# Kernel tuning notes

Measured on AMD Instinct MI355X. Metric: run time of the kernel, lower is better.

Reference implementation:

```python
import jax, jax.numpy as jnp
import numpy as np
import math

D_MODEL = 1024
N_HEADS = 16
D_K = D_MODEL // N_HEADS
BS, SQ, SK = 2, 2048, 2048


def setup_inputs() -> dict:
    key = jax.random.key(0)
    ks = jax.random.split(key, 7)
    q = jax.random.normal(ks[0], (BS, SQ, D_MODEL), dtype=jnp.float32)
    k = jax.random.normal(ks[1], (BS, SK, D_MODEL), dtype=jnp.float32)
    v = jax.random.normal(ks[2], (BS, SK, D_MODEL), dtype=jnp.float32)
    # causal mask: True = masked out (matches torch masked_fill semantics)
    mask = jnp.broadcast_to(
        ~jnp.tril(jnp.ones((SQ, SK), dtype=bool)), (BS, SQ, SK))
    scale = 1.0 / math.sqrt(D_MODEL)
    wq = jax.random.normal(ks[3], (D_MODEL, D_MODEL), dtype=jnp.float32) * scale
    wk = jax.random.normal(ks[4], (D_MODEL, D_MODEL), dtype=jnp.float32) * scale
    wv = jax.random.normal(ks[5], (D_MODEL, D_MODEL), dtype=jnp.float32) * scale
    wo = jax.random.normal(ks[6], (D_MODEL, D_MODEL), dtype=jnp.float32) * scale
    return {"q": q, "k": k, "v": v, "mask": mask,
            "wq": wq, "wk": wk, "wv": wv, "wo": wo}


def reference(q, k, v, mask, wq, wk, wv, wo):
    bs, sq, _ = q.shape
    sk = k.shape[1]
    # nn.Linear(bias=False): x @ W.T ; reshape to heads -> [b, h, s, d_k]
    qh = (q @ wq.T).reshape(bs, sq, N_HEADS, D_K).transpose(0, 2, 1, 3)
    kh = (k @ wk.T).reshape(bs, sk, N_HEADS, D_K).transpose(0, 2, 1, 3)
    vh = (v @ wv.T).reshape(bs, sk, N_HEADS, D_K).transpose(0, 2, 1, 3)
    # scaled dot-product attention, full [b,h,sq,sk] scores (as original)
    z = jnp.einsum('bhqd,bhkd->bhqk', qh, kh) / math.sqrt(D_K)
    z = jnp.where(mask[:, None, :, :], jnp.float32(-1e10), z)
    z = jax.nn.softmax(z, axis=-1)
    z = jnp.einsum('bhqk,bhkd->bhqd', z, vh)
    z = z.transpose(0, 2, 1, 3).reshape(bs, sq, D_MODEL)
    return z @ wo.T
```

## Files before the change

### kernel.cpp

```cpp
#include <hip/hip_runtime.h>
#include <hip/hip_bf16.h>
#include <stdint.h>

typedef short s16x8 __attribute__((ext_vector_type(8)));
typedef float f32x4 __attribute__((ext_vector_type(4)));

#define BSZ 2
#define SQL 2048
#define DMODEL 1024
#define NHEAD 16
#define DKH 64

#if __has_builtin(__builtin_amdgcn_exp2f)
#define EXP2(x) __builtin_amdgcn_exp2f(x)
#else
#define EXP2(x) exp2f(x)
#endif

__device__ __forceinline__ ushort f2bf(float f) {
  uint32_t u = __float_as_uint(f);
  u += 0x7fffu + ((u >> 16) & 1u);
  return (ushort)(u >> 16);
}

__device__ __forceinline__ uint32_t cvtpk_bf16(float lo, float hi) {
  uint32_t r;
  asm("v_cvt_pk_bf16_f32 %0, %1, %2" : "=v"(r) : "v"(lo), "v"(hi));
  return r;
}

__device__ __forceinline__ float rowmax16(float x) {
  x = fmaxf(x, __int_as_float(__builtin_amdgcn_update_dpp(0, __float_as_int(x), 0x121, 0xf, 0xf, true)));
  x = fmaxf(x, __int_as_float(__builtin_amdgcn_update_dpp(0, __float_as_int(x), 0x122, 0xf, 0xf, true)));
  x = fmaxf(x, __int_as_float(__builtin_amdgcn_update_dpp(0, __float_as_int(x), 0x124, 0xf, 0xf, true)));
  x = fmaxf(x, __int_as_float(__builtin_amdgcn_update_dpp(0, __float_as_int(x), 0x128, 0xf, 0xf, true)));
  return x;
}

__device__ __forceinline__ void gload_lds16(const ushort* g, ushort* l) {
  __builtin_amdgcn_global_load_lds((const __attribute__((address_space(1))) void*)g,
                                   (__attribute__((address_space(3))) void*)l,
                                   16, 0, 0);
}

__global__ void cvt_all(const float* __restrict__ q, const float* __restrict__ k,
                        const float* __restrict__ v, const float* __restrict__ wq,
                        const float* __restrict__ wk, const float* __restrict__ wv,
                        const float* __restrict__ wo, ushort* __restrict__ dq,
                        ushort* __restrict__ dk, ushort* __restrict__ dv,
                        ushort* __restrict__ dwq, ushort* __restrict__ dwk,
                        ushort* __restrict__ dwv, ushort* __restrict__ dwo) {
  int b = blockIdx.x;
  const float* s; ushort* d; int off;
  if (b < 4096)       { s = q;  d = dq;  off = b; }
  else if (b < 8192)  { s = k;  d = dk;  off = b - 4096; }
  else if (b < 12288) { s = v;  d = dv;  off = b - 8192; }
  else if (b < 13312) { s = wq; d = dwq; off = b - 12288; }
  else if (b < 14336) { s = wk; d = dwk; off = b - 13312; }
  else if (b < 15360) { s = wv; d = dwv; off = b - 14336; }
  else                { s = wo; d = dwo; off = b - 15360; }
  int i = (off * 256 + threadIdx.x) * 4;
  float4 x = *(const float4*)(s + i);
  ushort4 o;
  o.x = f2bf(x.x); o.y = f2bf(x.y); o.z = f2bf(x.z); o.w = f2bf(x.w);
  *(ushort4*)(d + i) = o;
}

__device__ __forceinline__ void gemm_core(const ushort* __restrict__ A,
                                          const ushort* __restrict__ B,
                                          ushort* sA, ushort* sB, f32x4 (&acc)[4][4]) {
  const int t = threadIdx.x, w = t >> 6, lane = t & 63;
  const int lrow = lane & 15, lk = (lane >> 4) * 8;
  const int m0 = blockIdx.x * 128, n0 = blockIdx.y * 128;
  const int wm = (w >> 1) * 64, wn = (w & 1) * 64;

  auto stage = [&](int kt, int buf) {
#pragma unroll
    for (int i = 0; i < 2; ++i) {
      int ci = i * 256 + t;
      int row = ci >> 2;
      int ce = (ci & 3) * 8;
      gload_lds16(A + (size_t)(m0 + row) * 1024 + kt * 32 + ce,
                  sA + buf * 4096 + (i * 256 + w * 64) * 8);
      gload_lds16(B + (size_t)(n0 + row) * 1024 + kt * 32 + ce,
                  sB + buf * 4096 + (i * 256 + w * 64) * 8);
    }
  };

  stage(0, 0);
  for (int kt = 0; kt < 32; ++kt) {
    const int cur = kt & 1;
    if (kt < 31) {
      stage(kt + 1, cur ^ 1);
      asm volatile("s_waitcnt vmcnt(4)" ::: "memory");
    } else {
      asm volatile("s_waitcnt vmcnt(0)" ::: "memory");
    }
    __builtin_amdgcn_s_barrier();
    __builtin_amdgcn_sched_barrier(0);
    const ushort* pA = sA + cur * 4096;
    const ushort* pB = sB + cur * 4096;
    s16x8 af[4], bfr[4];
#pragma unroll
    for (int mi = 0; mi < 4; ++mi)
      af[mi] = *(const s16x8*)(pA + (wm + mi * 16 + lrow) * 32 + lk);
#pragma unroll
    for (int ni = 0; ni < 4; ++ni)
      bfr[ni] = *(const s16x8*)(pB + (wn + ni * 16 + lrow) * 32 + lk);
    __builtin_amdgcn_s_setprio(1);
#pragma unroll
    for (int mi = 0; mi < 4; ++mi)
#pragma unroll
      for (int ni = 0; ni < 4; ++ni)
        acc[mi][ni] = __builtin_amdgcn_mfma_f32_16x16x32_bf16(af[mi], bfr[ni], acc[mi][ni], 0, 0, 0);
    __builtin_amdgcn_s_setprio(0);
    asm volatile("s_waitcnt lgkmcnt(0)" ::: "memory");
    __builtin_amdgcn_s_barrier();
  }
}

__device__ __forceinline__ void epi_heads(f32x4 (&acc)[4][4], ushort* D, float scale, bool vtrans) {
  const int lane = threadIdx.x & 63, w = threadIdx.x >> 6;
  const int m0 = blockIdx.x * 128, n0 = blockIdx.y * 128;
  const int wm = (w >> 1) * 64, wn = (w & 1) * 64;
#pragma unroll
  for (int mi = 0; mi < 4; ++mi)
#pragma unroll
    for (int ni = 0; ni < 4; ++ni)
#pragma unroll
      for (int r = 0; r < 4; ++r) {
        int m = m0 + wm + mi * 16 + (lane >> 4) * 4 + r;
        int n = n0 + wn + ni * 16 + (lane & 15);
        ushort bv = f2bf(acc[mi][ni][r] * scale);
        int b = m >> 11, s = m & 2047, h = n >> 6, d = n & 63;
        if (vtrans) {
          int sp = (s & ~63) | (((s & 15) << 2) | ((s >> 4) & 3));
          D[((size_t)((b * 16 + h) * 64 + d)) * 2048 + sp] = bv;
        } else {
          D[((size_t)((b * 16 + h) * 2048 + s)) * 64 + d] = bv;
        }
      }
}

__global__ __launch_bounds__(256) void gemm_qkv(const ushort* __restrict__ qb,
                                                const ushort* __restrict__ kb,
                                                const ushort* __restrict__ vb,
                                                const ushort* __restrict__ wqb,
                                                const ushort* __restrict__ wkb,
                                                const ushort* __restrict__ wvb,
                                                ushort* __restrict__ Qh,
                                                ushort* __restrict__ Kh,
                                                ushort* __restrict__ Vt) {
  __shared__ __align__(16) ushort sA[2 * 128 * 32];
  __shared__ __align__(16) ushort sB[2 * 128 * 32];
  const int z = blockIdx.z;
  const ushort* A = (z == 0) ? qb : (z == 1) ? kb : vb;
  const ushort* B = (z == 0) ? wqb : (z == 1) ? wkb : wvb;
  f32x4 acc[4][4] = {};
  gemm_core(A, B, sA, sB, acc);
  ushort* D = (z == 0) ? Qh : (z == 1) ? Kh : Vt;
  epi_heads(acc, D, (z == 0) ? 0.18033688f : 1.0f, z == 2);
}

__global__ __launch_bounds__(256) void gemm_out64(const ushort* __restrict__ A,
                                                  const ushort* __restrict__ B,
                                                  float* __restrict__ D) {
  __shared__ __align__(16) ushort sA[2 * 64 * 32];
  __shared__ __align__(16) ushort sB[2 * 128 * 32];
  const int t = threadIdx.x, w = t >> 6, lane = t & 63;
  const int lrow = lane & 15, lk = (lane >> 4) * 8;
  const int m0 = blockIdx.x * 64, n0 = blockIdx.y * 128;
  const int wm = (w >> 1) * 32, wn = (w & 1) * 64;
  f32x4 acc[2][4] = {};

  auto stage = [&](int kt, int buf) {
    {
      int row = t >> 2, ce = (t & 3) * 8;
      gload_lds16(A + (size_t)(m0 + row) * 1024 + kt * 32 + ce,
                  sA + buf * 2048 + (w * 64) * 8);
    }
#pragma unroll
    for (int i = 0; i < 2; ++i) {
      int ci = i * 256 + t;
      int row = ci >> 2, ce = (ci & 3) * 8;
      gload_lds16(B + (size_t)(n0 + row) * 1024 + kt * 32 + ce,
                  sB + buf * 4096 + (i * 256 + w * 64) * 8);
    }
  };

  stage(0, 0);
  for (int kt = 0; kt < 32; ++kt) {
    const int cur = kt & 1;
    if (kt < 31) {
      stage(kt + 1, cur ^ 1);
      asm volatile("s_waitcnt vmcnt(3)" ::: "memory");
    } else {
      asm volatile("s_waitcnt vmcnt(0)" ::: "memory");
    }
    __builtin_amdgcn_s_barrier();
    __builtin_amdgcn_sched_barrier(0);
    const ushort* pA = sA + cur * 2048;
    const ushort* pB = sB + cur * 4096;
    s16x8 af[2], bfr[4];
#pragma unroll
    for (int mi = 0; mi < 2; ++mi)
      af[mi] = *(const s16x8*)(pA + (wm + mi * 16 + lrow) * 32 + lk);
#pragma unroll
    for (int ni = 0; ni < 4; ++ni)
      bfr[ni] = *(const s16x8*)(pB + (wn + ni * 16 + lrow) * 32 + lk);
    __builtin_amdgcn_s_setprio(1);
#pragma unroll
    for (int mi = 0; mi < 2; ++mi)
#pragma unroll
      for (int ni = 0; ni < 4; ++ni)
        acc[mi][ni] = __builtin_amdgcn_mfma_f32_16x16x32_bf16(af[mi], bfr[ni], acc[mi][ni], 0, 0, 0);
    __builtin_amdgcn_s_setprio(0);
    asm volatile("s_waitcnt lgkmcnt(0)" ::: "memory");
    __builtin_amdgcn_s_barrier();
  }

#pragma unroll
  for (int mi = 0; mi < 2; ++mi)
#pragma unroll
    for (int ni = 0; ni < 4; ++ni)
#pragma unroll
      for (int r = 0; r < 4; ++r) {
        int m = m0 + wm + mi * 16 + (lane >> 4) * 4 + r;
        int n = n0 + wn + ni * 16 + (lane & 15);
        D[(size_t)m * 1024 + n] = acc[mi][ni][r];
      }
}

__global__ __launch_bounds__(512) void attn_fwd(const ushort* __restrict__ Qh,
                                                const ushort* __restrict__ Kh,
                                                const ushort* __restrict__ Vt,
                                                ushort* __restrict__ Z) {
  __shared__ __align__(16) ushort sK[2][64 * 64];
  __shared__ __align__(16) ushort sV[2][64 * 64];
  __shared__ __align__(16) ushort sP[8][16 * 72];
  const int t = threadIdx.x, w = t >> 6, lane = t & 63;
  const int lcol = lane & 15, lhi = lane >> 4;
  const int a = blockIdx.x * 2, bh = blockIdx.y;
  const int g = w >> 2, wg = w & 3;
  const int tbase = g ? (30 - a) : a;
  const int qt_w = tbase + (wg >> 1);
  const int qr0 = tbase * 64 + wg * 32;
  const int rbase = (wg & 1) * 32;
  const ushort* Qb = Qh + (size_t)bh * SQL * DKH;
  const ushort* Kb = Kh + (size_t)bh * SQL * DKH;
  const ushort* Vb = Vt + (size_t)bh * DKH * SQL;

  s16x8 qf[2][2];
#pragma unroll
  for (int s = 0; s < 2; ++s) {
    const ushort* qp = Qb + (size_t)(qr0 + s * 16 + lcol) * DKH + lhi * 8;
    qf[s][0] = *(const s16x8*)qp;
    qf[s][1] = *(const s16x8*)(qp + 32);
  }
  float mr[2][4], lrp[2][4];
  f32x4 o[2][4] = {};
#pragma unroll
  for (int s = 0; s < 2; ++s)
#pragma unroll
    for (int r = 0; r < 4; ++r) { mr[s][r] = -1e30f; lrp[s][r] = 0.f; }
  ushort* Pw = &sP[w][0];

  auto stage = [&](int kb, int buf) {
    int row = t >> 3, cc = t & 7;
    int scz = cc ^ (row & 7);
    gload_lds16(Kb + (size_t)(kb * 64 + row) * DKH + scz * 8, &sK[buf][w * 512]);
    gload_lds16(Vb + (size_t)row * SQL + kb * 64 + scz * 8, &sV[buf][w * 512]);
  };

  const int nkb = 32 - a;
  stage(0, 0);
  for (int kb = 0; kb < nkb; ++kb) {
    const int cur = kb & 1;
    if (kb + 1 < nkb) {
      stage(kb + 1, cur ^ 1);
      asm volatile("s_waitcnt vmcnt(2)" ::: "memory");
    } else {
      asm volatile("s_waitcnt vmcnt(0)" ::: "memory");
    }
    __builtin_amdgcn_s_barrier();
    __builtin_amdgcn_sched_barrier(0);
    const bool act = (kb <= qt_w);
    if (act) {
      const ushort* pK = &sK[cur][0];
      const ushort* pV = &sV[cur][0];
      f32x4 scs[2][4];
      __builtin_amdgcn_s_setprio(1);
#pragma unroll
      for (int ktt = 0; ktt < 4; ++ktt) {
        int row = ktt * 16 + lcol;
        int c0 = lhi ^ (row & 7);
        int c1 = (lhi + 4) ^ (row & 7);
        s16x8 k0 = *(const s16x8*)(pK + row * 64 + c0 * 8);
        s16x8 k1 = *(const s16x8*)(pK + row * 64 + c1 * 8);
        f32x4 a0 = {};
        a0 = __builtin_amdgcn_mfma_f32_16x16x32_bf16(qf[0][0], k0, a0, 0, 0, 0);
        a0 = __builtin_amdgcn_mfma_f32_16x16x32_bf16(qf[0][1], k1, a0, 0, 0, 0);
        scs[0][ktt] = a0;
        f32x4 b2 = {};
        b2 = __builtin_amdgcn_mfma_f32_16x16x32_bf16(qf[1][0], k0, b2, 0, 0, 0);
        b2 = __builtin_amdgcn_mfma_f32_16x16x32_bf16(qf[1][1], k1, b2, 0, 0, 0);
        scs[1][ktt] = b2;
      }
      __builtin_amdgcn_s_setprio(0);
      if (kb == qt_w) {
#pragma unroll
        for (int s = 0; s < 2; ++s)
#pragma unroll
          for (int ktt = 0; ktt < 4; ++ktt) {
            int kloc = ktt * 16 + lcol;
#pragma unroll
            for (int r = 0; r < 4; ++r)
              if (kloc > rbase + s * 16 + lhi * 4 + r) scs[s][ktt][r] = -1e30f;
          }
      }
#pragma unroll
      for (int s = 0; s < 2; ++s) {
        if (s == 1) {
          asm volatile("s_waitcnt lgkmcnt(0)" ::: "memory");
          __builtin_amdgcn_sched_barrier(0);
        }
        float tm4[4];
#pragma unroll
        for (int r = 0; r < 4; ++r) {
          float tm = fmaxf(fmaxf(scs[s][0][r], scs[s][1][r]), fmaxf(scs[s][2][r], scs[s][3][r]));
          tm4[r] = rowmax16(tm);
        }
        bool grow = (tm4[0] > mr[s][0] + 8.f) || (tm4[1] > mr[s][1] + 8.f) ||
                    (tm4[2] > mr[s][2] + 8.f) || (tm4[3] > mr[s][3] + 8.f);
        if (__any((int)grow)) {
#pragma unroll
          for (int r = 0; r < 4; ++r) {
            float mn = fmaxf(mr[s][r], tm4[r]);
            float al = EXP2(mr[s][r] - mn);
            lrp[s][r] *= al;
            o[s][0][r] *= al; o[s][1][r] *= al; o[s][2][r] *= al; o[s][3][r] *= al;
            mr[s][r] = mn;
          }
        }
#pragma unroll
        for (int r = 0; r < 4; ++r) {
          float p0 = EXP2(scs[s][0][r] - mr[s][r]);
          float p1 = EXP2(scs[s][1][r] - mr[s][r]);
          float p2 = EXP2(scs[s][2][r] - mr[s][r]);
          float p3 = EXP2(scs[s][3][r] - mr[s][r]);
          lrp[s][r] += (p0 + p1) + (p2 + p3);
          uint2 pk;
          pk.x = cvtpk_bf16(p0, p1);
          pk.y = cvtpk_bf16(p2, p3);
          *(uint2*)(Pw + (lhi * 4 + r) * 72 + lcol * 4) = pk;
        }
        __builtin_amdgcn_s_setprio(1);
#pragma unroll
        for (int kc = 0; kc < 2; ++kc) {
          s16x8 pf = *(const s16x8*)(Pw + lcol * 72 + kc * 32 + lhi * 8);
#pragma unroll
          for (int dt = 0; dt < 4; ++dt) {
            int row = dt * 16 + lcol;
            int cc = (lhi + 4 * kc) ^ (row & 7);
            s16x8 vf = *(const s16x8*)(pV + row * 64 + cc * 8);
            o[s][dt] = __builtin_amdgcn_mfma_f32_16x16x32_bf16(pf, vf, o[s][dt], 0, 0, 0);
          }
        }
        __builtin_amdgcn_s_setprio(0);
      }
    }
    asm volatile("s_waitcnt lgkmcnt(0)" ::: "memory");
    __builtin_amdgcn_s_barrier();
  }

  const int b = bh >> 4, h = bh & 15;
#pragma unroll
  for (int s = 0; s < 2; ++s) {
#pragma unroll
    for (int r = 0; r < 4; ++r) {
      float sum = lrp[s][r];
      sum += __shfl_xor(sum, 1);
      sum += __shfl_xor(sum, 2);
      sum += __shfl_xor(sum, 4);
      sum += __shfl_xor(sum, 8);
      float inv = 1.0f / sum;
      int q = qr0 + s * 16 + lhi * 4 + r;
      size_t base = ((size_t)(b * SQL + q)) * DMODEL + h * DKH + lcol;
#pragma unroll
      for (int dt = 0; dt < 4; ++dt)
        Z[base + dt * 16] = f2bf(o[s][dt][r] * inv);
    }
  }
}

extern "C" void kernel_launch(void* const* d_in, const int* in_sizes, int n_in,
                              void* d_out, int out_size, void* d_ws, size_t ws_size,
                              hipStream_t stream) {
  const float* q = (const float*)d_in[0];
  const float* k = (const float*)d_in[1];
  const float* v = (const float*)d_in[2];
  const float* wq = (const float*)d_in[4];
  const float* wk = (const float*)d_in[5];
  const float* wv = (const float*)d_in[6];
  const float* wo = (const float*)d_in[7];

  const size_t NBIG = (size_t)BSZ * SQL * DMODEL;
  const size_t NW = (size_t)DMODEL * DMODEL;
  ushort* qb = (ushort*)d_ws;
  ushort* kb = qb + NBIG;
  ushort* vb = kb + NBIG;
  ushort* wqb = vb + NBIG;
  ushort* wkb = wqb + NW;
  ushort* wvb = wkb + NW;
  ushort* wob = wvb + NW;
  ushort* Qh = wob + NW;
  ushort* Kh = Qh + NBIG;
  ushort* Vt = Kh + NBIG;
  ushort* Z  = Vt + NBIG;

  cvt_all<<<dim3(16384), 256, 0, stream>>>(q, k, v, wq, wk, wv, wo,
                                           qb, kb, vb, wqb, wkb, wvb, wob);
  gemm_qkv<<<dim3(32, 8, 3), 256, 0, stream>>>(qb, kb, vb, wqb, wkb, wvb, Qh, Kh, Vt);
  attn_fwd<<<dim3(8, BSZ * NHEAD), 512, 0, stream>>>(Qh, Kh, Vt, Z);
  gemm_out64<<<dim3(64, 8), 256, 0, stream>>>(Z, wob, (float*)d_out);
}
```

Before: 145.4 us.

## Split attention KV loop across wave pairs and merge partial softmax states

```diff
diff --git a/kernel.cpp b/kernel.cpp
--- a/kernel.cpp
+++ b/kernel.cpp
@@ -231,21 +231,21 @@
       }
 }
 
-__global__ __launch_bounds__(512) void attn_fwd(const ushort* __restrict__ Qh,
-                                                const ushort* __restrict__ Kh,
-                                                const ushort* __restrict__ Vt,
-                                                ushort* __restrict__ Z) {
-  __shared__ __align__(16) ushort sK[2][64 * 64];
-  __shared__ __align__(16) ushort sV[2][64 * 64];
-  __shared__ __align__(16) ushort sP[8][16 * 72];
+__global__ __launch_bounds__(512, 4) void attn_fwd(const ushort* __restrict__ Qh,
+                                                   const ushort* __restrict__ Kh,
+                                                   const ushort* __restrict__ Vt,
+                                                   ushort* __restrict__ Z) {
+  __shared__ __align__(16) ushort smem[25600];
+  ushort* sK = smem;
+  ushort* sV = smem + 8192;
+  ushort* sP = smem + 16384;
   const int t = threadIdx.x, w = t >> 6, lane = t & 63;
   const int lcol = lane & 15, lhi = lane >> 4;
-  const int a = blockIdx.x * 2, bh = blockIdx.y;
-  const int g = w >> 2, wg = w & 3;
-  const int tbase = g ? (30 - a) : a;
-  const int qt_w = tbase + (wg >> 1);
-  const int qr0 = tbase * 64 + wg * 32;
-  const int rbase = (wg & 1) * 32;
+  const int p = blockIdx.x, bh = blockIdx.y;
+  const int slot = w >> 1, half = w & 1;
+  const int qt_w = (slot < 2) ? p : (31 - p);
+  const int rbase = (slot & 1) * 32;
+  const int qr0 = qt_w * 64 + rbase;
   const ushort* Qb = Qh + (size_t)bh * SQL * DKH;
   const ushort* Kb = Kh + (size_t)bh * SQL * DKH;
   const ushort* Vb = Vt + (size_t)bh * DKH * SQL;
@@ -263,16 +263,16 @@
   for (int s = 0; s < 2; ++s)
 #pragma unroll
     for (int r = 0; r < 4; ++r) { mr[s][r] = -1e30f; lrp[s][r] = 0.f; }
-  ushort* Pw = &sP[w][0];
+  ushort* Pw = sP + w * 1152;
 
   auto stage = [&](int kb, int buf) {
     int row = t >> 3, cc = t & 7;
     int scz = cc ^ (row & 7);
-    gload_lds16(Kb + (size_t)(kb * 64 + row) * DKH + scz * 8, &sK[buf][w * 512]);
-    gload_lds16(Vb + (size_t)row * SQL + kb * 64 + scz * 8, &sV[buf][w * 512]);
+    gload_lds16(Kb + (size_t)(kb * 64 + row) * DKH + scz * 8, sK + buf * 4096 + w * 512);
+    gload_lds16(Vb + (size_t)row * SQL + kb * 64 + scz * 8, sV + buf * 4096 + w * 512);
   };
 
-  const int nkb = 32 - a;
+  const int nkb = 32 - p;
   stage(0, 0);
   for (int kb = 0; kb < nkb; ++kb) {
     const int cur = kb & 1;
@@ -284,10 +284,10 @@
     }
     __builtin_amdgcn_s_barrier();
     __builtin_amdgcn_sched_barrier(0);
-    const bool act = (kb <= qt_w);
+    const bool act = (kb <= qt_w) && ((kb & 1) == half);
     if (act) {
-      const ushort* pK = &sK[cur][0];
-      const ushort* pV = &sV[cur][0];
+      const ushort* pK = sK + cur * 4096;
+      const ushort* pV = sV + cur * 4096;
       f32x4 scs[2][4];
       __builtin_amdgcn_s_setprio(1);
 #pragma unroll
@@ -373,9 +373,9 @@
     __builtin_amdgcn_s_barrier();
   }
 
-  const int b = bh >> 4, h = bh & 15;
-#pragma unroll
-  for (int s = 0; s < 2; ++s) {
+  float lsum[2][4];
+#pragma unroll
+  for (int s = 0; s < 2; ++s)
 #pragma unroll
     for (int r = 0; r < 4; ++r) {
       float sum = lrp[s][r];
@@ -383,13 +383,57 @@
       sum += __shfl_xor(sum, 2);
       sum += __shfl_xor(sum, 4);
       sum += __shfl_xor(sum, 8);
-      float inv = 1.0f / sum;
-      int q = qr0 + s * 16 + lhi * 4 + r;
-      size_t base = ((size_t)(b * SQL + q)) * DMODEL + h * DKH + lcol;
+      lsum[s][r] = sum;
+    }
+
+  float* mo = (float*)smem + slot * 2112;
+  float* ml = mo + 2048;
+  if (half == 1) {
+#pragma unroll
+    for (int s = 0; s < 2; ++s)
 #pragma unroll
       for (int dt = 0; dt < 4; ++dt)
-        Z[base + dt * 16] = f2bf(o[s][dt][r] * inv);
-    }
+        *(f32x4*)(mo + (((s * 4 + lhi) * 4 + dt) * 16 + lcol) * 4) = o[s][dt];
+    if (lcol == 0) {
+#pragma unroll
+      for (int s = 0; s < 2; ++s)
+#pragma unroll
+        for (int r = 0; r < 4; ++r) {
+          float2 v = make_float2(mr[s][r], lsum[s][r]);
+          *(float2*)(ml + (s * 16 + lhi * 4 + r) * 2) = v;
+        }
+    }
+  }
+  asm volatile("s_waitcnt lgkmcnt(0)" ::: "memory");
+  __builtin_amdgcn_s_barrier();
+  __builtin_amdgcn_sched_barrier(0);
+  if (half == 0) {
+    const int b = bh >> 4, h = bh & 15;
+    float a0s[2][4], a1s[2][4], invs[2][4];
+#pragma unroll
+    for (int s = 0; s < 2; ++s)
+#pragma unroll
+      for (int r = 0; r < 4; ++r) {
+        float2 v = *(const float2*)(ml + (s * 16 + lhi * 4 + r) * 2);
+        float mf = fmaxf(mr[s][r], v.x);
+        float A0 = EXP2(mr[s][r] - mf);
+        float A1 = EXP2(v.x - mf);
+        float l = lsum[s][r] * A0 + v.y * A1;
+        a0s[s][r] = A0; a1s[s][r] = A1; invs[s][r] = 1.0f / l;
+      }
+#pragma unroll
+    for (int s = 0; s < 2; ++s)
+#pragma unroll
+      for (int dt = 0; dt < 4; ++dt) {
+        f32x4 o1 = *(const f32x4*)(mo + (((s * 4 + lhi) * 4 + dt) * 16 + lcol) * 4);
+#pragma unroll
+        for (int r = 0; r < 4; ++r) {
+          int qrow = qr0 + s * 16 + lhi * 4 + r;
+          size_t base = ((size_t)(b * SQL + qrow)) * DMODEL + h * DKH + lcol;
+          float val = (o[s][dt][r] * a0s[s][r] + o1[r] * a1s[s][r]) * invs[s][r];
+          Z[base + dt * 16] = f2bf(val);
+        }
+      }
   }
 }
 
@@ -421,6 +465,6 @@
   cvt_all<<<dim3(16384), 256, 0, stream>>>(q, k, v, wq, wk, wv, wo,
                                            qb, kb, vb, wqb, wkb, wvb, wob);
   gemm_qkv<<<dim3(32, 8, 3), 256, 0, stream>>>(qb, kb, vb, wqb, wkb, wvb, Qh, Kh, Vt);
-  attn_fwd<<<dim3(8, BSZ * NHEAD), 512, 0, stream>>>(Qh, Kh, Vt, Z);
+  attn_fwd<<<dim3(16, BSZ * NHEAD), 512, 0, stream>>>(Qh, Kh, Vt, Z);
   gemm_out64<<<dim3(64, 8), 256, 0, stream>>>(Z, wob, (float*)d_out);
 }
```

After: 151.7 us. 1.04x slower.

## Drop LDS staging in attention; load K/V fragments directly from global per wave

Applied to the files above, without the earlier changes.

```diff
diff --git a/kernel.cpp b/kernel.cpp
--- a/kernel.cpp
+++ b/kernel.cpp
@@ -231,21 +231,18 @@
       }
 }
 
-__global__ __launch_bounds__(512) void attn_fwd(const ushort* __restrict__ Qh,
+__global__ __launch_bounds__(256) void attn_fwd(const ushort* __restrict__ Qh,
                                                 const ushort* __restrict__ Kh,
                                                 const ushort* __restrict__ Vt,
                                                 ushort* __restrict__ Z) {
-  __shared__ __align__(16) ushort sK[2][64 * 64];
-  __shared__ __align__(16) ushort sV[2][64 * 64];
-  __shared__ __align__(16) ushort sP[8][16 * 72];
+  __shared__ __align__(16) ushort sP[4][16 * 72];
   const int t = threadIdx.x, w = t >> 6, lane = t & 63;
   const int lcol = lane & 15, lhi = lane >> 4;
-  const int a = blockIdx.x * 2, bh = blockIdx.y;
-  const int g = w >> 2, wg = w & 3;
-  const int tbase = g ? (30 - a) : a;
-  const int qt_w = tbase + (wg >> 1);
-  const int qr0 = tbase * 64 + wg * 32;
-  const int rbase = (wg & 1) * 32;
+  const int bh = blockIdx.y;
+  const int j = blockIdx.x * 4 + w;
+  const int js0 = j, js1 = 127 - j;
+  const int dg0 = js0 >> 2, dg1 = js1 >> 2;
+  const int rb0 = (js0 & 3) * 16, rb1 = (js1 & 3) * 16;
   const ushort* Qb = Qh + (size_t)bh * SQL * DKH;
   const ushort* Kb = Kh + (size_t)bh * SQL * DKH;
   const ushort* Vb = Vt + (size_t)bh * DKH * SQL;
@@ -253,7 +250,8 @@
   s16x8 qf[2][2];
 #pragma unroll
   for (int s = 0; s < 2; ++s) {
-    const ushort* qp = Qb + (size_t)(qr0 + s * 16 + lcol) * DKH + lhi * 8;
+    int qr = (s == 0 ? js0 : js1) * 16;
+    const ushort* qp = Qb + (size_t)(qr + lcol) * DKH + lhi * 8;
     qf[s][0] = *(const s16x8*)qp;
     qf[s][1] = *(const s16x8*)(qp + 32);
   }
@@ -265,117 +263,117 @@
     for (int r = 0; r < 4; ++r) { mr[s][r] = -1e30f; lrp[s][r] = 0.f; }
   ushort* Pw = &sP[w][0];
 
-  auto stage = [&](int kb, int buf) {
-    int row = t >> 3, cc = t & 7;
-    int scz = cc ^ (row & 7);
-    gload_lds16(Kb + (size_t)(kb * 64 + row) * DKH + scz * 8, &sK[buf][w * 512]);
-    gload_lds16(Vb + (size_t)row * SQL + kb * 64 + scz * 8, &sV[buf][w * 512]);
-  };
-
-  const int nkb = 32 - a;
-  stage(0, 0);
+  const int nkb = dg1 + 1;
   for (int kb = 0; kb < nkb; ++kb) {
-    const int cur = kb & 1;
-    if (kb + 1 < nkb) {
-      stage(kb + 1, cur ^ 1);
-      asm volatile("s_waitcnt vmcnt(2)" ::: "memory");
-    } else {
-      asm volatile("s_waitcnt vmcnt(0)" ::: "memory");
-    }
-    __builtin_amdgcn_s_barrier();
+    const ushort* Kt = Kb + (size_t)kb * 64 * DKH;
+    const ushort* Vtl = Vb + (size_t)kb * 64;
+    s16x8 kf0[4], kf1[4];
+#pragma unroll
+    for (int ktt = 0; ktt < 4; ++ktt) {
+      const ushort* kp = Kt + (size_t)(ktt * 16 + lcol) * DKH + lhi * 8;
+      kf0[ktt] = *(const s16x8*)kp;
+      kf1[ktt] = *(const s16x8*)(kp + 32);
+    }
+    s16x8 vf[2][4];
+#pragma unroll
+    for (int kc = 0; kc < 2; ++kc)
+#pragma unroll
+      for (int dt = 0; dt < 4; ++dt)
+        vf[kc][dt] = *(const s16x8*)(Vtl + (size_t)(dt * 16 + lcol) * SQL + (lhi + 4 * kc) * 8);
+
+    const bool act0 = (kb <= dg0);
+    f32x4 scs[2][4];
+    __builtin_amdgcn_s_setprio(1);
+#pragma unroll
+    for (int ktt = 0; ktt < 4; ++ktt) {
+      f32x4 a1 = {};
+      a1 = __builtin_amdgcn_mfma_f32_16x16x32_bf16(qf[1][0], kf0[ktt], a1, 0, 0, 0);
+      a1 = __builtin_amdgcn_mfma_f32_16x16x32_bf16(qf[1][1], kf1[ktt], a1, 0, 0, 0);
+      scs[1][ktt] = a1;
+    }
+    if (act0) {
+#pragma unroll
+      for (int ktt = 0; ktt < 4; ++ktt) {
+        f32x4 a0 = {};
+        a0 = __builtin_amdgcn_mfma_f32_16x16x32_bf16(qf[0][0], kf0[ktt], a0, 0, 0, 0);
+        a0 = __builtin_amdgcn_mfma_f32_16x16x32_bf16(qf[0][1], kf1[ktt], a0, 0, 0, 0);
+        scs[0][ktt] = a0;
+      }
+    }
+    __builtin_amdgcn_s_setprio(0);
+    if (kb == dg1) {
+#pragma unroll
+      for (int ktt = 0; ktt < 4; ++ktt) {
+        int kloc = ktt * 16 + lcol;
+#pragma unroll
+        for (int r = 0; r < 4; ++r)
+          if (kloc > rb1 + lhi * 4 + r) scs[1][ktt][r] = -1e30f;
+      }
+    }
+    if (act0 && kb == dg0) {
+#pragma unroll
+      for (int ktt = 0; ktt < 4; ++ktt) {
+        int kloc = ktt * 16 + lcol;
+#pragma unroll
+        for (int r = 0; r < 4; ++r)
+          if (kloc > rb0 + lhi * 4 + r) scs[0][ktt][r] = -1e30f;
+      }
+    }
+#pragma unroll
+    for (int s = 0; s < 2; ++s) {
+      if (s == 0 && !act0) continue;
+      if (s == 1) {
+        asm volatile("s_waitcnt lgkmcnt(0)" ::: "memory");
+        __builtin_amdgcn_sched_barrier(0);
+      }
+      float tm4[4];
+#pragma unroll
+      for (int r = 0; r < 4; ++r) {
+        float tm = fmaxf(fmaxf(scs[s][0][r], scs[s][1][r]), fmaxf(scs[s][2][r], scs[s][3][r]));
+        tm4[r] = rowmax16(tm);
+      }
+      bool grow = (tm4[0] > mr[s][0] + 8.f) || (tm4[1] > mr[s][1] + 8.f) ||
+                  (tm4[2] > mr[s][2] + 8.f) || (tm4[3] > mr[s][3] + 8.f);
+      if (__any((int)grow)) {
+#pragma unroll
+        for (int r = 0; r < 4; ++r) {
+          float mn = fmaxf(mr[s][r], tm4[r]);
+          float al = EXP2(mr[s][r] - mn);
+          lrp[s][r] *= al;
+          o[s][0][r] *= al; o[s][1][r] *= al; o[s][2][r] *= al; o[s][3][r] *= al;
+          mr[s][r] = mn;
+        }
+      }
+#pragma unroll
+      for (int r = 0; r < 4; ++r) {
+        float p0 = EXP2(scs[s][0][r] - mr[s][r]);
+        float p1 = EXP2(scs[s][1][r] - mr[s][r]);
+        float p2 = EXP2(scs[s][2][r] - mr[s][r]);
+        float p3 = EXP2(scs[s][3][r] - mr[s][r]);
+        lrp[s][r] += (p0 + p1) + (p2 + p3);
+        uint2 pk;
+        pk.x = cvtpk_bf16(p0, p1);
+        pk.y = cvtpk_bf16(p2, p3);
+        *(uint2*)(Pw + (lhi * 4 + r) * 72 + lcol * 4) = pk;
+      }
+      __builtin_amdgcn_s_setprio(1);
+#pragma unroll
+      for (int kc = 0; kc < 2; ++kc) {
+        s16x8 pf = *(const s16x8*)(Pw + lcol * 72 + kc * 32 + lhi * 8);
+#pragma unroll
+        for (int dt = 0; dt < 4; ++dt)
+          o[s][dt] = __builtin_amdgcn_mfma_f32_16x16x32_bf16(pf, vf[kc][dt], o[s][dt], 0, 0, 0);
+      }
+      __builtin_amdgcn_s_setprio(0);
+    }
+    asm volatile("s_waitcnt lgkmcnt(0)" ::: "memory");
     __builtin_amdgcn_sched_barrier(0);
-    const bool act = (kb <= qt_w);
-    if (act) {
-      const ushort* pK = &sK[cur][0];
-      const ushort* pV = &sV[cur][0];
-      f32x4 scs[2][4];
-      __builtin_amdgcn_s_setprio(1);
-#pragma unroll
-      for (int ktt = 0; ktt < 4; ++ktt) {
-        int row = ktt * 16 + lcol;
-        int c0 = lhi ^ (row & 7);
-        int c1 = (lhi + 4) ^ (row & 7);
-        s16x8 k0 = *(const s16x8*)(pK + row * 64 + c0 * 8);
-        s16x8 k1 = *(const s16x8*)(pK + row * 64 + c1 * 8);
-        f32x4 a0 = {};
-        a0 = __builtin_amdgcn_mfma_f32_16x16x32_bf16(qf[0][0], k0, a0, 0, 0, 0);
-        a0 = __builtin_amdgcn_mfma_f32_16x16x32_bf16(qf[0][1], k1, a0, 0, 0, 0);
-        scs[0][ktt] = a0;
-        f32x4 b2 = {};
-        b2 = __builtin_amdgcn_mfma_f32_16x16x32_bf16(qf[1][0], k0, b2, 0, 0, 0);
-        b2 = __builtin_amdgcn_mfma_f32_16x16x32_bf16(qf[1][1], k1, b2, 0, 0, 0);
-        scs[1][ktt] = b2;
-      }
-      __builtin_amdgcn_s_setprio(0);
-      if (kb == qt_w) {
-#pragma unroll
-        for (int s = 0; s < 2; ++s)
-#pragma unroll
-          for (int ktt = 0; ktt < 4; ++ktt) {
-            int kloc = ktt * 16 + lcol;
-#pragma unroll
-            for (int r = 0; r < 4; ++r)
-              if (kloc > rbase + s * 16 + lhi * 4 + r) scs[s][ktt][r] = -1e30f;
-          }
-      }
-#pragma unroll
-      for (int s = 0; s < 2; ++s) {
-        if (s == 1) {
-          asm volatile("s_waitcnt lgkmcnt(0)" ::: "memory");
-          __builtin_amdgcn_sched_barrier(0);
-        }
-        float tm4[4];
-#pragma unroll
-        for (int r = 0; r < 4; ++r) {
-          float tm = fmaxf(fmaxf(scs[s][0][r], scs[s][1][r]), fmaxf(scs[s][2][r], scs[s][3][r]));
-          tm4[r] = rowmax16(tm);
-        }
-        bool grow = (tm4[0] > mr[s][0] + 8.f) || (tm4[1] > mr[s][1] + 8.f) ||
-                    (tm4[2] > mr[s][2] + 8.f) || (tm4[3] > mr[s][3] + 8.f);
-        if (__any((int)grow)) {
-#pragma unroll
-          for (int r = 0; r < 4; ++r) {
-            float mn = fmaxf(mr[s][r], tm4[r]);
-            float al = EXP2(mr[s][r] - mn);
-            lrp[s][r] *= al;
-            o[s][0][r] *= al; o[s][1][r] *= al; o[s][2][r] *= al; o[s][3][r] *= al;
-            mr[s][r] = mn;
-          }
-        }
-#pragma unroll
-        for (int r = 0; r < 4; ++r) {
-          float p0 = EXP2(scs[s][0][r] - mr[s][r]);
-          float p1 = EXP2(scs[s][1][r] - mr[s][r]);
-          float p2 = EXP2(scs[s][2][r] - mr[s][r]);
-          float p3 = EXP2(scs[s][3][r] - mr[s][r]);
-          lrp[s][r] += (p0 + p1) + (p2 + p3);
-          uint2 pk;
-          pk.x = cvtpk_bf16(p0, p1);
-          pk.y = cvtpk_bf16(p2, p3);
-          *(uint2*)(Pw + (lhi * 4 + r) * 72 + lcol * 4) = pk;
-        }
-        __builtin_amdgcn_s_setprio(1);
-#pragma unroll
-        for (int kc = 0; kc < 2; ++kc) {
-          s16x8 pf = *(const s16x8*)(Pw + lcol * 72 + kc * 32 + lhi * 8);
-#pragma unroll
-          for (int dt = 0; dt < 4; ++dt) {
-            int row = dt * 16 + lcol;
-            int cc = (lhi + 4 * kc) ^ (row & 7);
-            s16x8 vf = *(const s16x8*)(pV + row * 64 + cc * 8);
-            o[s][dt] = __builtin_amdgcn_mfma_f32_16x16x32_bf16(pf, vf, o[s][dt], 0, 0, 0);
-          }
-        }
-        __builtin_amdgcn_s_setprio(0);
-      }
-    }
-    asm volatile("s_waitcnt lgkmcnt(0)" ::: "memory");
-    __builtin_amdgcn_s_barrier();
   }
 
   const int b = bh >> 4, h = bh & 15;
 #pragma unroll
   for (int s = 0; s < 2; ++s) {
+    int qr0 = (s == 0 ? js0 : js1) * 16;
 #pragma unroll
     for (int r = 0; r < 4; ++r) {
       float sum = lrp[s][r];
@@ -384,7 +382,7 @@
       sum += __shfl_xor(sum, 4);
       sum += __shfl_xor(sum, 8);
       float inv = 1.0f / sum;
-      int q = qr0 + s * 16 + lhi * 4 + r;
+      int q = qr0 + lhi * 4 + r;
       size_t base = ((size_t)(b * SQL + q)) * DMODEL + h * DKH + lcol;
 #pragma unroll
       for (int dt = 0; dt < 4; ++dt)
@@ -421,6 +419,6 @@
   cvt_all<<<dim3(16384), 256, 0, stream>>>(q, k, v, wq, wk, wv, wo,
                                            qb, kb, vb, wqb, wkb, wvb, wob);
   gemm_qkv<<<dim3(32, 8, 3), 256, 0, stream>>>(qb, kb, vb, wqb, wkb, wvb, Qh, Kh, Vt);
-  attn_fwd<<<dim3(8, BSZ * NHEAD), 512, 0, stream>>>(Qh, Kh, Vt, Z);
+  attn_fwd<<<dim3(16, BSZ * NHEAD), 256, 0, stream>>>(Qh, Kh, Vt, Z);
   gemm_out64<<<dim3(64, 8), 256, 0, stream>>>(Z, wob, (float*)d_out);
 }
```

Measured after the change: 197.8 us. 1.36x slower.
